# Performance work log

Measured on AMD Instinct MI355X. Metric: run time of the kernel, lower is better.

Reference implementation:

```python
import jax, jax.numpy as jnp
import numpy as np

B, M, W, D = 256, 96, 128, 512

def setup_inputs() -> dict:
    key = jax.random.key(0)
    ks = jax.random.split(key, 12)
    s = 0.02
    return {
        "memory": jax.random.normal(ks[0], (B, M, D), dtype=jnp.float32),
        "write_tokens": jax.random.normal(ks[1], (B, W, D), dtype=jnp.float32),
        "Wq": jax.random.normal(ks[2], (D, D), dtype=jnp.float32) * s,
        "bq": jnp.zeros((D,), dtype=jnp.float32),
        "Wk": jax.random.normal(ks[3], (D, D), dtype=jnp.float32) * s,
        "bk": jnp.zeros((D,), dtype=jnp.float32),
        "We": jax.random.normal(ks[4], (D, D), dtype=jnp.float32) * s,
        "be": jnp.zeros((D,), dtype=jnp.float32),
        "Wa": jax.random.normal(ks[5], (D, D), dtype=jnp.float32) * s,
        "ba": jnp.zeros((D,), dtype=jnp.float32),
        "gamma": jnp.ones((D,), dtype=jnp.float32),
        "beta": jnp.zeros((D,), dtype=jnp.float32),
    }


def reference(memory, write_tokens, Wq, bq, Wk, bk, We, be, Wa, ba, gamma, beta):
    d = memory.shape[-1]
    scale = 1.0 / jnp.sqrt(jnp.asarray(d, dtype=memory.dtype))
    # QK attention: queries from write tokens, keys from memory
    q = write_tokens @ Wq.T + bq              # [B, W, D]
    k = memory @ Wk.T + bk                    # [B, M, D]
    scores = jnp.einsum('bwd,bmd->bwm', q, k) * scale
    attn = jax.nn.softmax(scores, axis=-1)    # [B, W, M]
    erase = jax.nn.sigmoid(write_tokens @ We.T + be)  # [B, W, D]
    add = jnp.tanh(write_tokens @ Wa.T + ba)          # [B, W, D]

    # sequential erase/add loop over write tokens (faithful to torch loop)
    def step(mem, inp):
        a, e, ad = inp  # a: [B, M], e/ad: [B, D]
        mem = mem * (1.0 - a[:, :, None] * e[:, None, :]) + a[:, :, None] * ad[:, None, :]
        return mem, None

    xs = (jnp.swapaxes(attn, 0, 1), jnp.swapaxes(erase, 0, 1), jnp.swapaxes(add, 0, 1))
    new_memory, _ = jax.lax.scan(step, memory, xs)

    # LayerNorm over embedding dim (eps=1e-5); dropout is identity in eval
    mu = jnp.mean(new_memory, axis=-1, keepdims=True)
    var = jnp.mean(jnp.square(new_memory - mu), axis=-1, keepdims=True)
    out = (new_memory - mu) * jax.lax.rsqrt(var + 1e-5) * gamma + beta
    return out
```

## Files before the change

### kernel.cpp

```cpp
#include <hip/hip_runtime.h>
#include <cstdint>
#include <cstddef>

#define B_ 256
#define M_ 96
#define W_ 128
#define D_ 512

typedef _Float16 f16;
typedef __attribute__((ext_vector_type(8))) _Float16 f16x8;
typedef __attribute__((ext_vector_type(2))) _Float16 f16x2;
typedef __attribute__((ext_vector_type(4))) float f32x4;

typedef __attribute__((address_space(3))) void lds_void;
typedef const __attribute__((address_space(1))) void glb_void;

__device__ __forceinline__ void gload_lds16(const void* g, void* l) {
  __builtin_amdgcn_global_load_lds((glb_void*)g, (lds_void*)l, 16, 0, 0);
}

__global__ void cvt_f32_f16(const float* __restrict__ in, f16* __restrict__ out, int n8) {
  int i = blockIdx.x * 256 + threadIdx.x;
  if (i >= n8) return;
  const float4* p = (const float4*)in + (size_t)i * 2;
  float4 a = p[0], b = p[1];
  f16x8 o = { (f16)a.x, (f16)a.y, (f16)a.z, (f16)a.w,
              (f16)b.x, (f16)b.y, (f16)b.z, (f16)b.w };
  ((f16x8*)out)[i] = o;
}

template<int MODE>
__global__ __launch_bounds__(256, 2)
void gemm_bt(const f16* __restrict__ A, const f16* __restrict__ Bm,
             const float* __restrict__ bias,
             f16* __restrict__ out0, f16* __restrict__ out1, f16* __restrict__ out2)
{
  constexpr int K = 512;
  constexpr int BK = 64;
  __shared__ f16 As[128 * BK];
  __shared__ f16 Bs[128 * BK];
  const int tid = threadIdx.x;
  const int lane = tid & 63;
  const int wv = tid >> 6;
  const int wr = wv >> 1, wc = wv & 1;
  const int bm = blockIdx.x, bn = blockIdx.y;
  const f16* Ab = A + (size_t)bm * 128 * K;
  const f16* Bb = Bm + (size_t)bn * 128 * K;

  f32x4 acc[4][4] = {};

  const int r0 = tid >> 3;
  const int c0 = (tid & 7) * 8;

  for (int kk = 0; kk < K / BK; ++kk) {
    const int kbase = kk * BK;
#pragma unroll
    for (int p = 0; p < 4; ++p) {
      int row = p * 32 + r0;
      gload_lds16(Ab + (size_t)row * K + kbase + c0, As + row * BK + c0);
    }
#pragma unroll
    for (int p = 0; p < 4; ++p) {
      int row = p * 32 + r0;
      gload_lds16(Bb + (size_t)row * K + kbase + c0, Bs + row * BK + c0);
    }
    __syncthreads();
#pragma unroll
    for (int ks = 0; ks < 2; ++ks) {
      const int ko = ks * 32 + (lane >> 4) * 8;
      f16x8 af[4], bf[4];
#pragma unroll
      for (int i = 0; i < 4; ++i)
        af[i] = *(const f16x8*)(As + (wr * 64 + i * 16 + (lane & 15)) * BK + ko);
#pragma unroll
      for (int i = 0; i < 4; ++i)
        bf[i] = *(const f16x8*)(Bs + (wc * 64 + i * 16 + (lane & 15)) * BK + ko);
#pragma unroll
      for (int i = 0; i < 4; ++i)
#pragma unroll
        for (int j = 0; j < 4; ++j)
          acc[i][j] = __builtin_amdgcn_mfma_f32_16x16x32_f16(af[i], bf[j], acc[i][j], 0, 0, 0);
    }
    __syncthreads();
  }

  const int er = (lane >> 4) * 4;
  const int ec = lane & 15;
#pragma unroll
  for (int i = 0; i < 4; ++i) {
#pragma unroll
    for (int j = 0; j < 4; ++j) {
      const int gc = bn * 128 + wc * 64 + j * 16 + ec;
      const float bv = bias[gc];
      const size_t rbase = (size_t)(bm * 128 + wr * 64 + i * 16 + er);
      if (MODE == 0) {
#pragma unroll
        for (int r = 0; r < 4; ++r) {
          float v = acc[i][j][r] + bv;
          out0[(rbase + r) * D_ + gc] = (f16)v;
        }
      } else {
        const int seg = gc >> 9;
        const int cc = gc & 511;
#pragma unroll
        for (int r = 0; r < 4; ++r) {
          float v = acc[i][j][r] + bv;
          if (seg == 0) {
            out0[(rbase + r) * D_ + cc] = (f16)v;
          } else if (seg == 1) {
            float s = __builtin_amdgcn_rcpf(1.f + __expf(-v));
            out1[(rbase + r) * D_ + cc] = (f16)s;
          } else {
            float vc = fminf(fmaxf(v, -15.f), 15.f);
            float t = __expf(2.f * vc);
            float th = (t - 1.f) * __builtin_amdgcn_rcpf(t + 1.f);
            out2[(rbase + r) * D_ + cc] = (f16)th;
          }
        }
      }
    }
  }
}

__global__ __launch_bounds__(256, 2)
void scores_softmax(const f16* __restrict__ q16, const f16* __restrict__ k16,
                    float* __restrict__ attn)
{
  __shared__ f16 Qs[64 * 64];
  __shared__ f16 Ks[96 * 64];
  const int b = blockIdx.x;
  const int wt = blockIdx.y;
  const int tid = threadIdx.x, lane = tid & 63, wv = tid >> 6;
  const f16* Qb = q16 + ((size_t)b * W_ + wt * 64) * D_;
  const f16* Kb = k16 + (size_t)b * M_ * D_;
  f32x4 acc[6] = {};
  const int r0 = tid >> 3, c0 = (tid & 7) * 8;

  for (int kk = 0; kk < 8; ++kk) {
    const int kbase = kk * 64;
#pragma unroll
    for (int p = 0; p < 2; ++p) {
      int row = p * 32 + r0;
      gload_lds16(Qb + (size_t)row * D_ + kbase + c0, Qs + row * 64 + c0);
    }
#pragma unroll
    for (int p = 0; p < 3; ++p) {
      int row = p * 32 + r0;
      gload_lds16(Kb + (size_t)row * D_ + kbase + c0, Ks + row * 64 + c0);
    }
    __syncthreads();
#pragma unroll
    for (int ks = 0; ks < 2; ++ks) {
      const int ko = ks * 32 + (lane >> 4) * 8;
      f16x8 aq = *(const f16x8*)(Qs + (wv * 16 + (lane & 15)) * 64 + ko);
#pragma unroll
      for (int j = 0; j < 6; ++j) {
        f16x8 bk8 = *(const f16x8*)(Ks + (j * 16 + (lane & 15)) * 64 + ko);
        acc[j] = __builtin_amdgcn_mfma_f32_16x16x32_f16(aq, bk8, acc[j], 0, 0, 0);
      }
    }
    __syncthreads();
  }

  const float scale = 0.04419417382415922f;
  const int er = (lane >> 4) * 4, ec = lane & 15;
#pragma unroll
  for (int r = 0; r < 4; ++r) {
    const int row = wt * 64 + wv * 16 + er + r;
    float s[6];
    float mx = -1e30f;
#pragma unroll
    for (int j = 0; j < 6; ++j) { s[j] = acc[j][r] * scale; mx = fmaxf(mx, s[j]); }
#pragma unroll
    for (int o = 1; o < 16; o <<= 1) mx = fmaxf(mx, __shfl_xor(mx, o));
    float sum = 0.f;
#pragma unroll
    for (int j = 0; j < 6; ++j) { s[j] = __expf(s[j] - mx); sum += s[j]; }
#pragma unroll
    for (int o = 1; o < 16; o <<= 1) sum += __shfl_xor(sum, o);
    const float inv = 1.f / sum;
#pragma unroll
    for (int j = 0; j < 6; ++j)
      attn[((size_t)b * W_ + row) * M_ + j * 16 + ec] = s[j] * inv;
  }
}

__global__ __launch_bounds__(256, 2)
void scan_ln(const float* __restrict__ memory, const f16* __restrict__ e16,
             const f16* __restrict__ a16, const float* __restrict__ attn,
             const float* __restrict__ gamma, const float* __restrict__ beta,
             float* __restrict__ out)
{
  __shared__ float a_s[32 * 32];
  __shared__ float red[32 * 8];
  __shared__ float mu_s[32], rs_s[32];
  const int blk = blockIdx.x;
  const int swz = (blk & 7) * 96 + (blk >> 3);
  const int b = swz / 3, mt = (swz % 3) * 32;
  const int tid = threadIdx.x;
  const int d0 = tid * 2;

  float2 acc[32];
  const float* memb = memory + ((size_t)b * M_ + mt) * D_ + d0;
#pragma unroll
  for (int m = 0; m < 32; ++m) acc[m] = *(const float2*)(memb + (size_t)m * D_);

  const f16* eb = e16 + (size_t)b * W_ * D_ + d0;
  const f16* ab = a16 + (size_t)b * W_ * D_ + d0;
  const float* atb = attn + (size_t)b * W_ * M_ + mt;

  for (int wch = 0; wch < 4; ++wch) {
    __syncthreads();
    {
      const int rr = tid >> 5, cc = tid & 31;
#pragma unroll
      for (int j = 0; j < 4; ++j) {
        int w = rr + 8 * j;
        a_s[w * 32 + cc] = atb[(size_t)(wch * 32 + w) * M_ + cc];
      }
    }
    __syncthreads();
    for (int wi = 0; wi < 32; ++wi) {
      const int w = wch * 32 + wi;
      f16x2 ev = *(const f16x2*)(eb + (size_t)w * D_);
      f16x2 av2 = *(const f16x2*)(ab + (size_t)w * D_);
      float ex = (float)ev.x, ey = (float)ev.y;
      float ax = (float)av2.x, ay = (float)av2.y;
      const float4* ap = (const float4*)(a_s + wi * 32);
      float aw[32];
#pragma unroll
      for (int j = 0; j < 8; ++j) {
        float4 t = ap[j];
        aw[4 * j] = t.x; aw[4 * j + 1] = t.y; aw[4 * j + 2] = t.z; aw[4 * j + 3] = t.w;
      }
#pragma unroll
      for (int m = 0; m < 32; ++m) {
        float a = aw[m];
        acc[m].x = fmaf(acc[m].x, fmaf(-a, ex, 1.f), a * ax);
        acc[m].y = fmaf(acc[m].y, fmaf(-a, ey, 1.f), a * ay);
      }
    }
  }

  const int lane = tid & 63, wv = tid >> 6;
#pragma unroll
  for (int m = 0; m < 32; ++m) {
    float s = acc[m].x + acc[m].y;
    float q = acc[m].x * acc[m].x + acc[m].y * acc[m].y;
#pragma unroll
    for (int o = 1; o < 64; o <<= 1) { s += __shfl_xor(s, o); q += __shfl_xor(q, o); }
    if (lane == 0) { red[m * 8 + wv] = s; red[m * 8 + 4 + wv] = q; }
  }
  __syncthreads();
  if (tid < 32) {
    float s = red[tid * 8] + red[tid * 8 + 1] + red[tid * 8 + 2] + red[tid * 8 + 3];
    float q = red[tid * 8 + 4] + red[tid * 8 + 5] + red[tid * 8 + 6] + red[tid * 8 + 7];
    float mu = s * (1.f / 512.f);
    float var = q * (1.f / 512.f) - mu * mu;
    mu_s[tid] = mu;
    rs_s[tid] = rsqrtf(var + 1e-5f);
  }
  __syncthreads();
  const float gx = gamma[d0], gy = gamma[d0 + 1];
  const float bx = beta[d0], by = beta[d0 + 1];
  float* ob = out + ((size_t)b * M_ + mt) * D_ + d0;
#pragma unroll
  for (int m = 0; m < 32; ++m) {
    float mu = mu_s[m], rs = rs_s[m];
    float2 o;
    o.x = (acc[m].x - mu) * rs * gx + bx;
    o.y = (acc[m].y - mu) * rs * gy + by;
    *(float2*)(ob + (size_t)m * D_) = o;
  }
}

extern "C" void kernel_launch(void* const* d_in, const int* in_sizes, int n_in,
                              void* d_out, int out_size, void* d_ws, size_t ws_size,
                              hipStream_t stream)
{
  const float* memory = (const float*)d_in[0];
  const float* wtok   = (const float*)d_in[1];
  const float* Wq = (const float*)d_in[2];
  const float* bq = (const float*)d_in[3];
  const float* Wk = (const float*)d_in[4];
  const float* bk = (const float*)d_in[5];
  const float* We = (const float*)d_in[6];
  const float* ba_e = (const float*)d_in[7];
  const float* Wa = (const float*)d_in[8];
  const float* ba_a = (const float*)d_in[9];
  const float* gamma = (const float*)d_in[10];
  const float* beta  = (const float*)d_in[11];
  float* out = (float*)d_out;

  uint8_t* ws = (uint8_t*)d_ws;
  size_t off = 0;
  auto alloc = [&](size_t bytes) -> void* {
    void* p = ws + off;
    off += (bytes + 255) & ~(size_t)255;
    return p;
  };
  f16* wt16   = (f16*)alloc((size_t)B_ * W_ * D_ * 2);
  f16* mem16  = (f16*)alloc((size_t)B_ * M_ * D_ * 2);
  f16* wqea16 = (f16*)alloc((size_t)3 * D_ * D_ * 2);
  f16* wk16   = (f16*)alloc((size_t)D_ * D_ * 2);
  f16* q16    = (f16*)alloc((size_t)B_ * W_ * D_ * 2);
  f16* k16    = (f16*)alloc((size_t)B_ * M_ * D_ * 2);
  f16* e16    = (f16*)alloc((size_t)B_ * W_ * D_ * 2);
  f16* a16    = (f16*)alloc((size_t)B_ * W_ * D_ * 2);
  float* attn = (float*)alloc((size_t)B_ * W_ * M_ * 4);
  float* bqea = (float*)alloc(3 * D_ * 4);
  (void)ws_size; (void)in_sizes; (void)n_in; (void)out_size;

  hipMemcpyAsync(bqea,            bq,   D_ * 4, hipMemcpyDeviceToDevice, stream);
  hipMemcpyAsync(bqea + D_,       ba_e, D_ * 4, hipMemcpyDeviceToDevice, stream);
  hipMemcpyAsync(bqea + 2 * D_,   ba_a, D_ * 4, hipMemcpyDeviceToDevice, stream);

  const int n8wt = B_ * W_ * D_ / 8;
  const int n8m  = B_ * M_ * D_ / 8;
  const int n8w  = D_ * D_ / 8;
  cvt_f32_f16<<<n8wt / 256, 256, 0, stream>>>(wtok, wt16, n8wt);
  cvt_f32_f16<<<n8m / 256, 256, 0, stream>>>(memory, mem16, n8m);
  cvt_f32_f16<<<n8w / 256, 256, 0, stream>>>(Wq, wqea16, n8w);
  cvt_f32_f16<<<n8w / 256, 256, 0, stream>>>(We, wqea16 + (size_t)D_ * D_, n8w);
  cvt_f32_f16<<<n8w / 256, 256, 0, stream>>>(Wa, wqea16 + (size_t)2 * D_ * D_, n8w);
  cvt_f32_f16<<<n8w / 256, 256, 0, stream>>>(Wk, wk16, n8w);

  gemm_bt<1><<<dim3(B_ * W_ / 128, 12), 256, 0, stream>>>(wt16, wqea16, bqea, q16, e16, a16);
  gemm_bt<0><<<dim3(B_ * M_ / 128, 4), 256, 0, stream>>>(mem16, wk16, bk, k16, nullptr, nullptr);
  scores_softmax<<<dim3(B_, 2), 256, 0, stream>>>(q16, k16, attn);
  scan_ln<<<dim3(B_ * 3), 256, 0, stream>>>(memory, e16, a16, attn, gamma, beta, out);
}
```

Before: 419.8 us.

## Merge conversion launches, drop bias memcpys, and restructure scan with scalar attn loads

Measured after the change: 379.9 us. 9.5% less time.

```diff
diff --git a/kernel.cpp b/kernel.cpp
--- a/kernel.cpp
+++ b/kernel.cpp
@@ -11,6 +11,7 @@
 typedef __attribute__((ext_vector_type(8))) _Float16 f16x8;
 typedef __attribute__((ext_vector_type(2))) _Float16 f16x2;
 typedef __attribute__((ext_vector_type(4))) float f32x4;
+typedef __attribute__((ext_vector_type(16))) float f32x16;
 
 typedef __attribute__((address_space(3))) void lds_void;
 typedef const __attribute__((address_space(1))) void glb_void;
@@ -19,9 +20,25 @@
   __builtin_amdgcn_global_load_lds((glb_void*)g, (lds_void*)l, 16, 0, 0);
 }
 
-__global__ void cvt_f32_f16(const float* __restrict__ in, f16* __restrict__ out, int n8) {
-  int i = blockIdx.x * 256 + threadIdx.x;
-  if (i >= n8) return;
+__device__ __forceinline__ void sload_rows2(const float* p, f32x16& a, f32x16& b) {
+  asm volatile(
+      "s_load_dwordx16 %0, %2, 0x0\n\t"
+      "s_load_dwordx16 %1, %2, 0x180"
+      : "=s"(a), "=s"(b)
+      : "s"(p));
+}
+__device__ __forceinline__ void swait2(f32x16& a, f32x16& b) {
+  asm volatile("s_waitcnt lgkmcnt(0)" : "+s"(a), "+s"(b));
+}
+
+__global__ void cvt_act(const float* __restrict__ wtok, f16* __restrict__ wt16,
+                        const float* __restrict__ mem, f16* __restrict__ mem16) {
+  const int bid = blockIdx.x;
+  const float* in;
+  f16* out;
+  int i;
+  if (bid < 8192) { in = wtok; out = wt16; i = bid * 256 + threadIdx.x; }
+  else            { in = mem;  out = mem16; i = (bid - 8192) * 256 + threadIdx.x; }
   const float4* p = (const float4*)in + (size_t)i * 2;
   float4 a = p[0], b = p[1];
   f16x8 o = { (f16)a.x, (f16)a.y, (f16)a.z, (f16)a.w,
@@ -29,10 +46,25 @@
   ((f16x8*)out)[i] = o;
 }
 
+__global__ void cvt_w(const float* __restrict__ w0, const float* __restrict__ w1,
+                      const float* __restrict__ w2, const float* __restrict__ w3,
+                      f16* __restrict__ out) {
+  const int bid = blockIdx.x;
+  const int g = bid >> 7;
+  const int il = (bid & 127) * 256 + threadIdx.x;
+  const float* src = (g == 0) ? w0 : (g == 1) ? w1 : (g == 2) ? w2 : w3;
+  const float4* p = (const float4*)src + (size_t)il * 2;
+  float4 a = p[0], b = p[1];
+  f16x8 o = { (f16)a.x, (f16)a.y, (f16)a.z, (f16)a.w,
+              (f16)b.x, (f16)b.y, (f16)b.z, (f16)b.w };
+  ((f16x8*)out)[(size_t)g * 32768 + il] = o;
+}
+
 template<int MODE>
 __global__ __launch_bounds__(256, 2)
 void gemm_bt(const f16* __restrict__ A, const f16* __restrict__ Bm,
-             const float* __restrict__ bias,
+             const float* __restrict__ bias0, const float* __restrict__ bias1,
+             const float* __restrict__ bias2,
              f16* __restrict__ out0, f16* __restrict__ out1, f16* __restrict__ out2)
 {
   constexpr int K = 512;
@@ -91,9 +123,9 @@
 #pragma unroll
     for (int j = 0; j < 4; ++j) {
       const int gc = bn * 128 + wc * 64 + j * 16 + ec;
-      const float bv = bias[gc];
       const size_t rbase = (size_t)(bm * 128 + wr * 64 + i * 16 + er);
       if (MODE == 0) {
+        const float bv = bias0[gc];
 #pragma unroll
         for (int r = 0; r < 4; ++r) {
           float v = acc[i][j][r] + bv;
@@ -102,6 +134,8 @@
       } else {
         const int seg = gc >> 9;
         const int cc = gc & 511;
+        const float* bp = (seg == 0) ? bias0 : (seg == 1) ? bias1 : bias2;
+        const float bv = bp[cc];
 #pragma unroll
         for (int r = 0; r < 4; ++r) {
           float v = acc[i][j][r] + bv;
@@ -185,74 +219,77 @@
   }
 }
 
-__global__ __launch_bounds__(256, 2)
+__global__ __launch_bounds__(256, 6)
 void scan_ln(const float* __restrict__ memory, const f16* __restrict__ e16,
              const f16* __restrict__ a16, const float* __restrict__ attn,
              const float* __restrict__ gamma, const float* __restrict__ beta,
              float* __restrict__ out)
 {
-  __shared__ float a_s[32 * 32];
-  __shared__ float red[32 * 8];
-  __shared__ float mu_s[32], rs_s[32];
+  __shared__ float red[16 * 8];
+  __shared__ float mu_s[16], rs_s[16];
   const int blk = blockIdx.x;
-  const int swz = (blk & 7) * 96 + (blk >> 3);
-  const int b = swz / 3, mt = (swz % 3) * 32;
+  const int swz = (blk & 7) * 192 + (blk >> 3);
+  const int b = swz / 6, mt = (swz % 6) * 16;
   const int tid = threadIdx.x;
   const int d0 = tid * 2;
 
-  float2 acc[32];
+  float2 acc[16];
   const float* memb = memory + ((size_t)b * M_ + mt) * D_ + d0;
 #pragma unroll
-  for (int m = 0; m < 32; ++m) acc[m] = *(const float2*)(memb + (size_t)m * D_);
+  for (int m = 0; m < 16; ++m) acc[m] = *(const float2*)(memb + (size_t)m * D_);
 
   const f16* eb = e16 + (size_t)b * W_ * D_ + d0;
   const f16* ab = a16 + (size_t)b * W_ * D_ + d0;
   const float* atb = attn + (size_t)b * W_ * M_ + mt;
 
-  for (int wch = 0; wch < 4; ++wch) {
-    __syncthreads();
-    {
-      const int rr = tid >> 5, cc = tid & 31;
-#pragma unroll
-      for (int j = 0; j < 4; ++j) {
-        int w = rr + 8 * j;
-        a_s[w * 32 + cc] = atb[(size_t)(wch * 32 + w) * M_ + cc];
-      }
-    }
-    __syncthreads();
-    for (int wi = 0; wi < 32; ++wi) {
-      const int w = wch * 32 + wi;
-      f16x2 ev = *(const f16x2*)(eb + (size_t)w * D_);
-      f16x2 av2 = *(const f16x2*)(ab + (size_t)w * D_);
-      float ex = (float)ev.x, ey = (float)ev.y;
-      float ax = (float)av2.x, ay = (float)av2.y;
-      const float4* ap = (const float4*)(a_s + wi * 32);
-      float aw[32];
-#pragma unroll
-      for (int j = 0; j < 8; ++j) {
-        float4 t = ap[j];
-        aw[4 * j] = t.x; aw[4 * j + 1] = t.y; aw[4 * j + 2] = t.z; aw[4 * j + 3] = t.w;
-      }
-#pragma unroll
-      for (int m = 0; m < 32; ++m) {
-        float a = aw[m];
-        acc[m].x = fmaf(acc[m].x, fmaf(-a, ex, 1.f), a * ax);
-        acc[m].y = fmaf(acc[m].y, fmaf(-a, ey, 1.f), a * ay);
-      }
-    }
+  float2 ev0, av0, ev1, av1;
+  {
+    f16x2 e0 = *(const f16x2*)(eb);
+    f16x2 a0 = *(const f16x2*)(ab);
+    f16x2 e1 = *(const f16x2*)(eb + D_);
+    f16x2 a1 = *(const f16x2*)(ab + D_);
+    ev0 = { (float)e0.x, (float)e0.y }; av0 = { (float)a0.x, (float)a0.y };
+    ev1 = { (float)e1.x, (float)e1.y }; av1 = { (float)a1.x, (float)a1.y };
+  }
+
+  for (int w = 0; w < W_; w += 2) {
+    f32x16 r0, r1;
+    sload_rows2(atb + (size_t)w * M_, r0, r1);
+
+    const int wn = (w + 2 < W_) ? (w + 2) : (W_ - 2);
+    f16x2 e0 = *(const f16x2*)(eb + (size_t)wn * D_);
+    f16x2 a0 = *(const f16x2*)(ab + (size_t)wn * D_);
+    f16x2 e1 = *(const f16x2*)(eb + (size_t)(wn + 1) * D_);
+    f16x2 a1 = *(const f16x2*)(ab + (size_t)(wn + 1) * D_);
+
+    swait2(r0, r1);
+#pragma unroll
+    for (int m = 0; m < 16; ++m) {
+      float a = r0[m];
+      acc[m].x = fmaf(a, fmaf(-ev0.x, acc[m].x, av0.x), acc[m].x);
+      acc[m].y = fmaf(a, fmaf(-ev0.y, acc[m].y, av0.y), acc[m].y);
+    }
+#pragma unroll
+    for (int m = 0; m < 16; ++m) {
+      float a = r1[m];
+      acc[m].x = fmaf(a, fmaf(-ev1.x, acc[m].x, av1.x), acc[m].x);
+      acc[m].y = fmaf(a, fmaf(-ev1.y, acc[m].y, av1.y), acc[m].y);
+    }
+    ev0 = { (float)e0.x, (float)e0.y }; av0 = { (float)a0.x, (float)a0.y };
+    ev1 = { (float)e1.x, (float)e1.y }; av1 = { (float)a1.x, (float)a1.y };
   }
 
   const int lane = tid & 63, wv = tid >> 6;
 #pragma unroll
-  for (int m = 0; m < 32; ++m) {
+  for (int m = 0; m < 16; ++m) {
     float s = acc[m].x + acc[m].y;
-    float q = acc[m].x * acc[m].x + acc[m].y * acc[m].y;
+    float q = fmaf(acc[m].x, acc[m].x, acc[m].y * acc[m].y);
 #pragma unroll
     for (int o = 1; o < 64; o <<= 1) { s += __shfl_xor(s, o); q += __shfl_xor(q, o); }
     if (lane == 0) { red[m * 8 + wv] = s; red[m * 8 + 4 + wv] = q; }
   }
   __syncthreads();
-  if (tid < 32) {
+  if (tid < 16) {
     float s = red[tid * 8] + red[tid * 8 + 1] + red[tid * 8 + 2] + red[tid * 8 + 3];
     float q = red[tid * 8 + 4] + red[tid * 8 + 5] + red[tid * 8 + 6] + red[tid * 8 + 7];
     float mu = s * (1.f / 512.f);
@@ -265,7 +302,7 @@
   const float bx = beta[d0], by = beta[d0 + 1];
   float* ob = out + ((size_t)b * M_ + mt) * D_ + d0;
 #pragma unroll
-  for (int m = 0; m < 32; ++m) {
+  for (int m = 0; m < 16; ++m) {
     float mu = mu_s[m], rs = rs_s[m];
     float2 o;
     o.x = (acc[m].x - mu) * rs * gx + bx;
@@ -285,9 +322,9 @@
   const float* Wk = (const float*)d_in[4];
   const float* bk = (const float*)d_in[5];
   const float* We = (const float*)d_in[6];
-  const float* ba_e = (const float*)d_in[7];
+  const float* be = (const float*)d_in[7];
   const float* Wa = (const float*)d_in[8];
-  const float* ba_a = (const float*)d_in[9];
+  const float* ba = (const float*)d_in[9];
   const float* gamma = (const float*)d_in[10];
   const float* beta  = (const float*)d_in[11];
   float* out = (float*)d_out;
@@ -301,32 +338,22 @@
   };
   f16* wt16   = (f16*)alloc((size_t)B_ * W_ * D_ * 2);
   f16* mem16  = (f16*)alloc((size_t)B_ * M_ * D_ * 2);
-  f16* wqea16 = (f16*)alloc((size_t)3 * D_ * D_ * 2);
-  f16* wk16   = (f16*)alloc((size_t)D_ * D_ * 2);
+  f16* w16    = (f16*)alloc((size_t)4 * D_ * D_ * 2);
   f16* q16    = (f16*)alloc((size_t)B_ * W_ * D_ * 2);
   f16* k16    = (f16*)alloc((size_t)B_ * M_ * D_ * 2);
   f16* e16    = (f16*)alloc((size_t)B_ * W_ * D_ * 2);
   f16* a16    = (f16*)alloc((size_t)B_ * W_ * D_ * 2);
   float* attn = (float*)alloc((size_t)B_ * W_ * M_ * 4);
-  float* bqea = (float*)alloc(3 * D_ * 4);
   (void)ws_size; (void)in_sizes; (void)n_in; (void)out_size;
 
-  hipMemcpyAsync(bqea,            bq,   D_ * 4, hipMemcpyDeviceToDevice, stream);
-  hipMemcpyAsync(bqea + D_,       ba_e, D_ * 4, hipMemcpyDeviceToDevice, stream);
-  hipMemcpyAsync(bqea + 2 * D_,   ba_a, D_ * 4, hipMemcpyDeviceToDevice, stream);
-
-  const int n8wt = B_ * W_ * D_ / 8;
-  const int n8m  = B_ * M_ * D_ / 8;
-  const int n8w  = D_ * D_ / 8;
-  cvt_f32_f16<<<n8wt / 256, 256, 0, stream>>>(wtok, wt16, n8wt);
-  cvt_f32_f16<<<n8m / 256, 256, 0, stream>>>(memory, mem16, n8m);
-  cvt_f32_f16<<<n8w / 256, 256, 0, stream>>>(Wq, wqea16, n8w);
-  cvt_f32_f16<<<n8w / 256, 256, 0, stream>>>(We, wqea16 + (size_t)D_ * D_, n8w);
-  cvt_f32_f16<<<n8w / 256, 256, 0, stream>>>(Wa, wqea16 + (size_t)2 * D_ * D_, n8w);
-  cvt_f32_f16<<<n8w / 256, 256, 0, stream>>>(Wk, wk16, n8w);
-
-  gemm_bt<1><<<dim3(B_ * W_ / 128, 12), 256, 0, stream>>>(wt16, wqea16, bqea, q16, e16, a16);
-  gemm_bt<0><<<dim3(B_ * M_ / 128, 4), 256, 0, stream>>>(mem16, wk16, bk, k16, nullptr, nullptr);
+  f16* wqea16 = w16;
+  f16* wk16   = w16 + (size_t)3 * D_ * D_;
+
+  cvt_act<<<dim3(8192 + 6144), 256, 0, stream>>>(wtok, wt16, memory, mem16);
+  cvt_w<<<dim3(512), 256, 0, stream>>>(Wq, We, Wa, Wk, w16);
+
+  gemm_bt<1><<<dim3(B_ * W_ / 128, 12), 256, 0, stream>>>(wt16, wqea16, bq, be, ba, q16, e16, a16);
+  gemm_bt<0><<<dim3(B_ * M_ / 128, 4), 256, 0, stream>>>(mem16, wk16, bk, nullptr, nullptr, k16, nullptr, nullptr);
   scores_softmax<<<dim3(B_, 2), 256, 0, stream>>>(q16, k16, attn);
-  scan_ln<<<dim3(B_ * 3), 256, 0, stream>>>(memory, e16, a16, attn, gamma, beta, out);
-}
+  scan_ln<<<dim3(B_ * 6), 256, 0, stream>>>(memory, e16, a16, attn, gamma, beta, out);
+}
```
